# Kernel optimization log

Hardware: AMD Instinct MI355X
Metric: run time of the kernel (lower is better)

## Reference

```python
import jax, jax.numpy as jnp
import numpy as np
import math

STAGE_NUM = 5


def _l2norm(t, axis):
    return t / (1e-6 + jnp.linalg.norm(t, axis=axis, keepdims=True))


def setup_inputs() -> dict:
    key = jax.random.key(0)
    ks = jax.random.split(key, 6)
    b, n, c, h, w, k = 8, 5, 512, 32, 32, 64
    x = jax.random.normal(ks[0], (b, n, c, h, w), dtype=jnp.float32)
    mu = jax.random.normal(ks[1], (1, c, k), dtype=jnp.float32) * math.sqrt(2.0 / k)
    mu = _l2norm(mu, axis=1)
    # 1x1 convs init: normal(0, sqrt(2/(1*1*out_channels)))
    std = math.sqrt(2.0 / c)
    conv1_w = jax.random.normal(ks[2], (c, c), dtype=jnp.float32) * std  # [out,in]
    conv1_b = jnp.zeros((c,), dtype=jnp.float32)
    conv2_w = jax.random.normal(ks[3], (c, c), dtype=jnp.float32) * std
    bn_gamma = jnp.ones((c,), dtype=jnp.float32)
    bn_beta = jnp.zeros((c,), dtype=jnp.float32)
    return {"x": x, "mu": mu, "conv1_w": conv1_w, "conv1_b": conv1_b,
            "conv2_w": conv2_w, "bn_gamma": bn_gamma, "bn_beta": bn_beta}


def reference(x, mu, conv1_w, conv1_b, conv2_w, bn_gamma, bn_beta):
    b, n, c, h, w = x.shape
    xf = x.reshape(b * n, c, h, w)
    idn = xf
    # conv1: 1x1 conv with bias
    y = jnp.einsum('bchw,dc->bdhw', xf, conv1_w) + conv1_b[None, :, None, None]
    # [b, c, N] with N = n*h*w
    y = y.reshape(b, n, c, h, w).transpose(0, 2, 1, 3, 4).reshape(b, c, n * h * w)
    mu_b = jnp.broadcast_to(mu, (b, c, mu.shape[2]))
    z = None
    # EM iterations (no_grad in original; fwd-only so just compute)
    for _ in range(STAGE_NUM):
        z = jax.nn.softmax(jnp.einsum('bcn,bck->bnk', y, mu_b), axis=2)  # [b,N,k]
        z_ = z / (1e-6 + z.sum(axis=1, keepdims=True))
        mu_b = _l2norm(jnp.einsum('bcn,bnk->bck', y, z_), axis=1)
    # reconstruction: mu @ z^T -> [b,c,N]
    rec = jnp.einsum('bck,bnk->bcn', mu_b, z)
    rec = jax.nn.relu(rec.reshape(b, c, n, h, w))
    rec = rec.transpose(0, 2, 1, 3, 4).reshape(b * n, c, h, w)
    # conv2 (no bias) + BatchNorm (training-mode batch stats)
    y2 = jnp.einsum('bchw,dc->bdhw', rec, conv2_w)
    mean = y2.mean(axis=(0, 2, 3), keepdims=True)
    var = y2.var(axis=(0, 2, 3), keepdims=True)
    y2 = (y2 - mean) * jax.lax.rsqrt(var + 1e-5)
    y2 = y2 * bn_gamma[None, :, None, None] + bn_beta[None, :, None, None]
    out = jax.nn.relu(y2 + idn).reshape(b, n, c, h, w)
    return out, mu_b
```

## Files before the change

kernel.cpp:

```cpp
#include <hip/hip_runtime.h>
#include <math.h>

#define CH 512
#define K 64
#define BB 8
#define NIMG 5
#define HW 1024
#define NP 5120
#define BI 40

typedef __attribute__((ext_vector_type(8))) _Float16 f16x8;
typedef __attribute__((ext_vector_type(4))) _Float16 f16x4;
typedef __attribute__((ext_vector_type(4))) float f32x4;
typedef __attribute__((ext_vector_type(8))) short s16x8;

#define AS1 __attribute__((address_space(1)))
#define AS3 __attribute__((address_space(3)))

__device__ inline long mufrag_idx(int b, int c, int k) {
    int cc = c >> 5, l4 = (c >> 3) & 3, e = c & 7;
    int j = k >> 4, l15 = k & 15;
    int lane = l4 * 16 + l15;
    return ((long)b << 15) + (((cc * 4 + j) * 64 + lane) << 3) + e;
}

__global__ __launch_bounds__(256) void wconv(const float* __restrict__ w,
                                             _Float16* __restrict__ o)
{
    int i = blockIdx.x * 256 + threadIdx.x;
    o[i] = (_Float16)w[i];
}

__global__ __launch_bounds__(256) void transpose_f16(
    const float* __restrict__ in, _Float16* __restrict__ out, int P)
{
    __shared__ float tile[64][65];
    int t = threadIdx.x;
    int p0 = blockIdx.x * 64, c0 = blockIdx.y * 64;
    long ibase = (long)blockIdx.z * CH * P;
    long obase = (long)blockIdx.z * P * CH;
    int pl = t & 63, chh = t >> 6;
    #pragma unroll
    for (int i = 0; i < 16; ++i)
        tile[chh + i * 4][pl] = in[ibase + (long)(c0 + chh + i * 4) * P + p0 + pl];
    __syncthreads();
    int cc = t & 31, pr = t >> 5;
    #pragma unroll
    for (int i = 0; i < 8; ++i) {
        int p = pr + i * 8;
        _Float16 lo = (_Float16)tile[cc * 2][p];
        _Float16 hi = (_Float16)tile[cc * 2 + 1][p];
        unsigned lob = (unsigned)*(unsigned short*)&lo;
        unsigned hib = (unsigned)*(unsigned short*)&hi;
        *(unsigned*)&out[obase + (long)(p0 + p) * CH + c0 + cc * 2] = lob | (hib << 16);
    }
}

__global__ __launch_bounds__(256) void bcast_mu2(const float* __restrict__ mu_in,
                                                 float* __restrict__ mu_cur,
                                                 _Float16* __restrict__ muF)
{
    int i = blockIdx.x * 256 + threadIdx.x;
    float v = mu_in[i & 32767];
    mu_cur[i] = v;
    int b = i >> 15, ck = i & 32767, c = ck >> 6, k = ck & 63;
    muF[mufrag_idx(b, c, k)] = (_Float16)v;
}

__global__ __launch_bounds__(256) void conv_tile(
    const _Float16* __restrict__ Wh, const _Float16* __restrict__ inT,
    const float* __restrict__ bias, _Float16* __restrict__ y2h,
    _Float16* __restrict__ y16, _Float16* __restrict__ yT16, int mode)
{
    __shared__ _Float16 Wt[128 * 64];
    __shared__ _Float16 Xt[128 * 64];
    int t = threadIdx.x;
    int lane = t & 63, w = t >> 6;
    int l15 = lane & 15, l4 = lane >> 4;
    int wd = w & 1, wp = w >> 1;
    int sw = (blockIdx.x & 7) * 160 + (blockIdx.x >> 3);
    int px = sw & 7;
    int dy = (sw >> 3) & 3;
    int bi = sw >> 5;
    int d0 = dy * 128;
    int pl0 = px * 128;
    long prow0 = (long)bi * HW + pl0;
    int ci_row = lane >> 3;
    int colb_phys = (lane & 7) * 16;

    f32x4 acc[4][4];
    #pragma unroll
    for (int ai = 0; ai < 4; ++ai)
        #pragma unroll
        for (int bj = 0; bj < 4; ++bj) acc[ai][bj] = (f32x4){0.f, 0.f, 0.f, 0.f};

    for (int c0 = 0; c0 < CH; c0 += 64) {
        __syncthreads();
        #pragma unroll
        for (int i = 0; i < 4; ++i) {
            int row = w * 32 + i * 8 + ci_row;
            int cb = colb_phys ^ ((row & 7) << 4);
            const _Float16* srcW = Wh + (long)(d0 + row) * CH + c0 + (cb >> 1);
            const _Float16* srcX = inT + (prow0 + row) * (long)CH + c0 + (cb >> 1);
            __builtin_amdgcn_global_load_lds((const AS1 void*)srcW,
                (AS3 void*)&Wt[(w * 32 + i * 8) * 64], 16, 0, 0);
            __builtin_amdgcn_global_load_lds((const AS1 void*)srcX,
                (AS3 void*)&Xt[(w * 32 + i * 8) * 64], 16, 0, 0);
        }
        __syncthreads();
        #pragma unroll
        for (int kk = 0; kk < 2; ++kk) {
            f16x8 af[4], bf[4];
            #pragma unroll
            for (int ai = 0; ai < 4; ++ai) {
                int row = wd * 64 + ai * 16 + l15;
                int cb = (kk * 64 + l4 * 16) ^ ((row & 7) << 4);
                af[ai] = *(const f16x8*)((const char*)Wt + row * 128 + cb);
            }
            #pragma unroll
            for (int bj = 0; bj < 4; ++bj) {
                int row = wp * 64 + bj * 16 + l15;
                int cb = (kk * 64 + l4 * 16) ^ ((row & 7) << 4);
                bf[bj] = *(const f16x8*)((const char*)Xt + row * 128 + cb);
            }
            #pragma unroll
            for (int ai = 0; ai < 4; ++ai)
                #pragma unroll
                for (int bj = 0; bj < 4; ++bj)
                    acc[ai][bj] = __builtin_amdgcn_mfma_f32_16x16x32_f16(
                        af[ai], bf[bj], acc[ai][bj], 0, 0, 0);
        }
    }

    int b = bi / NIMG, n = bi % NIMG;
    if (mode == 0) {
        #pragma unroll
        for (int ai = 0; ai < 4; ++ai) {
            int dd = d0 + wd * 64 + ai * 16 + l4 * 4;
            float b0 = bias[dd], b1 = bias[dd + 1], b2 = bias[dd + 2], b3 = bias[dd + 3];
            #pragma unroll
            for (int bj = 0; bj < 4; ++bj) {
                int pb = n * HW + pl0 + wp * 64 + bj * 16 + l15;
                f16x4 pk = { (_Float16)(acc[ai][bj][0] + b0), (_Float16)(acc[ai][bj][1] + b1),
                             (_Float16)(acc[ai][bj][2] + b2), (_Float16)(acc[ai][bj][3] + b3) };
                *(f16x4*)&yT16[((long)b * NP + pb) * CH + dd] = pk;
                long yb = ((long)b * CH + dd) * NP + pb;
                y16[yb] = pk[0];
                y16[yb + NP] = pk[1];
                y16[yb + 2 * NP] = pk[2];
                y16[yb + 3 * NP] = pk[3];
            }
        }
    } else {
        long obase = (long)bi * CH * HW;
        #pragma unroll
        for (int ai = 0; ai < 4; ++ai) {
            int dd = d0 + wd * 64 + ai * 16 + l4 * 4;
            #pragma unroll
            for (int bj = 0; bj < 4; ++bj) {
                int p = pl0 + wp * 64 + bj * 16 + l15;
                long o = obase + (long)dd * HW + p;
                y2h[o] = (_Float16)acc[ai][bj][0];
                y2h[o + HW] = (_Float16)acc[ai][bj][1];
                y2h[o + 2 * HW] = (_Float16)acc[ai][bj][2];
                y2h[o + 3 * HW] = (_Float16)acc[ai][bj][3];
            }
        }
    }
}

__global__ __launch_bounds__(256) void bn_stats2(const _Float16* __restrict__ y2h,
                                                 float* __restrict__ stats,
                                                 float* __restrict__ statsq)
{
    int d = blockIdx.x;
    int t = threadIdx.x;
    float s = 0.f, q = 0.f;
    for (int bi = 0; bi < BI; ++bi) {
        const _Float16* p = y2h + (long)bi * CH * HW + (long)d * HW;
        f16x4 v = *(const f16x4*)&p[t * 4];
        float v0 = (float)v[0], v1 = (float)v[1], v2 = (float)v[2], v3 = (float)v[3];
        s += v0 + v1 + v2 + v3;
        q += v0 * v0 + v1 * v1 + v2 * v2 + v3 * v3;
    }
    #pragma unroll
    for (int off = 1; off < 64; off <<= 1) {
        s += __shfl_xor(s, off, 64);
        q += __shfl_xor(q, off, 64);
    }
    __shared__ float ps[8];
    int wv = t >> 6, ln = t & 63;
    if (ln == 0) { ps[wv] = s; ps[4 + wv] = q; }
    __syncthreads();
    if (t == 0) {
        stats[d]  = ps[0] + ps[1] + ps[2] + ps[3];
        statsq[d] = ps[4] + ps[5] + ps[6] + ps[7];
    }
}

__global__ __launch_bounds__(256) void stage_z_mfma(
    const _Float16* __restrict__ yT, const _Float16* __restrict__ muF,
    _Float16* __restrict__ zT, _Float16* __restrict__ z16,
    float* __restrict__ zsum, int writeZ)
{
    __shared__ float zred[256];
    int t = threadIdx.x;
    int w = t >> 6, lane = t & 63, l15 = lane & 15, l4 = lane >> 4;
    int p0 = blockIdx.x * 64 + w * 16;
    int b = blockIdx.y;
    const _Float16* mf = muF + ((long)b << 15);
    const _Float16* a0p = yT + ((long)b * NP + p0 + l15) * CH + l4 * 8;
    f32x4 acc[4];
    #pragma unroll
    for (int j = 0; j < 4; ++j) acc[j] = (f32x4){0.f, 0.f, 0.f, 0.f};
    #pragma unroll
    for (int cc = 0; cc < 16; ++cc) {
        f16x8 a0 = *(const f16x8*)(a0p + cc * 32);
        #pragma unroll
        for (int j = 0; j < 4; ++j) {
            f16x8 bj = *(const f16x8*)&mf[(((cc * 4 + j) * 64) + lane) * 8];
            acc[j] = __builtin_amdgcn_mfma_f32_16x16x32_f16(a0, bj, acc[j], 0, 0, 0);
        }
    }
    float zv[4][4];
    #pragma unroll
    for (int i = 0; i < 4; ++i) {
        float m = fmaxf(fmaxf(acc[0][i], acc[1][i]), fmaxf(acc[2][i], acc[3][i]));
        #pragma unroll
        for (int off = 1; off < 16; off <<= 1) m = fmaxf(m, __shfl_xor(m, off, 64));
        float e0 = __expf(acc[0][i] - m);
        float e1 = __expf(acc[1][i] - m);
        float e2 = __expf(acc[2][i] - m);
        float e3 = __expf(acc[3][i] - m);
        float s = e0 + e1 + e2 + e3;
        #pragma unroll
        for (int off = 1; off < 16; off <<= 1) s += __shfl_xor(s, off, 64);
        float inv = 1.f / s;
        zv[0][i] = e0 * inv; zv[1][i] = e1 * inv;
        zv[2][i] = e2 * inv; zv[3][i] = e3 * inv;
    }
    int prow = p0 + l4 * 4;
    long ztbase = (long)b * K * NP;
    #pragma unroll
    for (int j = 0; j < 4; ++j) {
        f16x4 pk = { (_Float16)zv[j][0], (_Float16)zv[j][1],
                     (_Float16)zv[j][2], (_Float16)zv[j][3] };
        *(f16x4*)&zT[ztbase + (long)(l15 + 16 * j) * NP + prow] = pk;
    }
    if (writeZ) {
        long zbase = (long)b * NP * K;
        #pragma unroll
        for (int j = 0; j < 4; ++j)
            #pragma unroll
            for (int i = 0; i < 4; ++i)
                z16[zbase + (long)(prow + i) * K + l15 + 16 * j] = (_Float16)zv[j][i];
    }
    float part[4];
    #pragma unroll
    for (int j = 0; j < 4; ++j) {
        part[j] = zv[j][0] + zv[j][1] + zv[j][2] + zv[j][3];
        part[j] += __shfl_xor(part[j], 16, 64);
        part[j] += __shfl_xor(part[j], 32, 64);
    }
    if (l4 == 0) {
        #pragma unroll
        for (int j = 0; j < 4; ++j) zred[w * 64 + l15 + 16 * j] = part[j];
    }
    __syncthreads();
    if (t < 64)
        atomicAdd(&zsum[b * 64 + t], zred[t] + zred[64 + t] + zred[128 + t] + zred[192 + t]);
}

__global__ __launch_bounds__(256) void stage_mu_mfma(
    const _Float16* __restrict__ y16, const _Float16* __restrict__ zT,
    float* __restrict__ macc)
{
    int t = threadIdx.x;
    int w = t >> 6, lane = t & 63, l15 = lane & 15, l4 = lane >> 4;
    int pc = blockIdx.x, ct = blockIdx.y, b = blockIdx.z;
    int c0 = ct * 128 + w * 32;
    int pbase = pc * 320;
    const _Float16* zrow = zT + (long)b * K * NP + (long)l15 * NP + l4 * 8;
    const _Float16* a0p = y16 + ((long)b * CH + c0 + l15) * NP + l4 * 8;
    const _Float16* a1p = y16 + ((long)b * CH + c0 + 16 + l15) * NP + l4 * 8;
    f32x4 acc[2][4];
    #pragma unroll
    for (int ci = 0; ci < 2; ++ci)
        #pragma unroll
        for (int j = 0; j < 4; ++j) acc[ci][j] = (f32x4){0.f, 0.f, 0.f, 0.f};
    for (int p0 = pbase; p0 < pbase + 320; p0 += 32) {
        f16x8 a0 = *(const f16x8*)(a0p + p0);
        f16x8 a1 = *(const f16x8*)(a1p + p0);
        #pragma unroll
        for (int j = 0; j < 4; ++j) {
            f16x8 bj = *(const f16x8*)(zrow + (long)(16 * j) * NP + p0);
            acc[0][j] = __builtin_amdgcn_mfma_f32_16x16x32_f16(a0, bj, acc[0][j], 0, 0, 0);
            acc[1][j] = __builtin_amdgcn_mfma_f32_16x16x32_f16(a1, bj, acc[1][j], 0, 0, 0);
        }
    }
    float* mp = macc + ((long)pc * BB + b) * K * CH;
    #pragma unroll
    for (int ci = 0; ci < 2; ++ci)
        #pragma unroll
        for (int j = 0; j < 4; ++j)
            *(f32x4*)&mp[(long)(l15 + 16 * j) * CH + c0 + ci * 16 + l4 * 4] = acc[ci][j];
}

__global__ __launch_bounds__(256) void mu_norm2(
    const float* __restrict__ macc, const float* __restrict__ zsum,
    float* __restrict__ mu_cur, _Float16* __restrict__ mu16,
    _Float16* __restrict__ muF)
{
    int gw = blockIdx.x * 4 + (threadIdx.x >> 6);
    int lane = threadIdx.x & 63;
    int b = gw >> 6, k = gw & 63;
    float v[8];
    float s = 0.f;
    #pragma unroll
    for (int ci = 0; ci < 8; ++ci) {
        int c = ci * 64 + lane;
        float a = 0.f;
        #pragma unroll
        for (int pcc = 0; pcc < 16; ++pcc)
            a += macc[(((long)pcc * BB + b) * K + k) * CH + c];
        v[ci] = a; s += a * a;
    }
    #pragma unroll
    for (int off = 1; off < 64; off <<= 1) s += __shfl_xor(s, off, 64);
    float d = 1e-6f + zsum[b * 64 + k];
    float scale = 1.f / (1e-6f * d + sqrtf(s));
    long mb = (long)b << 15;
    #pragma unroll
    for (int ci = 0; ci < 8; ++ci) {
        int c = ci * 64 + lane;
        float m = v[ci] * scale;
        mu_cur[mb + (long)c * K + k] = m;
        mu16[mb + (long)c * K + k] = (_Float16)m;
        muF[mufrag_idx(b, c, k)] = (_Float16)m;
    }
}

__global__ __launch_bounds__(256) void rec_mfma(
    const _Float16* __restrict__ z16, const _Float16* __restrict__ mu16,
    _Float16* __restrict__ recT)
{
    __shared__ _Float16 rt[64 * 80];
    int t = threadIdx.x;
    int w = t >> 6, lane = t & 63, l15 = lane & 15, l4 = lane >> 4;
    int p0 = blockIdx.x * 64, ct = blockIdx.y, b = blockIdx.z;
    const _Float16* zb = z16 + (long)b * NP * K;
    const _Float16* mb = mu16 + ((long)b << 15) + (long)(ct * 64 + w * 16 + l15) * K + l4 * 8;
    f32x4 acc[4];
    #pragma unroll
    for (int pj = 0; pj < 4; ++pj) acc[pj] = (f32x4){0.f, 0.f, 0.f, 0.f};
    #pragma unroll
    for (int kc = 0; kc < 64; kc += 32) {
        f16x8 bfr = *(const f16x8*)(mb + kc);
        #pragma unroll
        for (int pj = 0; pj < 4; ++pj) {
            f16x8 a = *(const f16x8*)(zb + (long)(p0 + pj * 16 + l15) * K + kc + l4 * 8);
            acc[pj] = __builtin_amdgcn_mfma_f32_16x16x32_f16(a, bfr, acc[pj], 0, 0, 0);
        }
    }
    #pragma unroll
    for (int pj = 0; pj < 4; ++pj)
        #pragma unroll
        for (int i = 0; i < 4; ++i)
            rt[(pj * 16 + l4 * 4 + i) * 80 + w * 16 + l15] = (_Float16)fmaxf(acc[pj][i], 0.f);
    __syncthreads();
    #pragma unroll
    for (int it = 0; it < 2; ++it) {
        int l = t + it * 256;
        int row = l >> 3, s8 = l & 7;
        *(s16x8*)&recT[((long)b * NP + p0 + row) * CH + ct * 64 + s8 * 8] =
            *(const s16x8*)&rt[row * 80 + s8 * 8];
    }
}

__global__ __launch_bounds__(256) void final_kernel(
    const _Float16* __restrict__ y2h, const float* __restrict__ x,
    const float* __restrict__ stats, const float* __restrict__ statsq,
    const float* __restrict__ gamma, const float* __restrict__ beta,
    const float* __restrict__ mu_cur, float* __restrict__ out)
{
    long i4 = (long)blockIdx.x * 256 + threadIdx.x;
    const long NMAIN4 = (long)BI * CH * HW / 4;
    if (i4 < NMAIN4) {
        long i = i4 * 4;
        int d = (int)((i >> 10) & (CH - 1));
        float s = stats[d], sq = statsq[d];
        const float inv = 1.f / (float)(BI * HW);
        float mean = s * inv;
        float var = sq * inv - mean * mean;
        float rs = rsqrtf(var + 1e-5f);
        float g = rs * gamma[d];
        float bb = beta[d] - mean * g;
        f16x4 yv = *(const f16x4*)&y2h[i];
        float4 xv = *(const float4*)&x[i];
        float4 ov;
        ov.x = fmaxf((float)yv[0] * g + bb + xv.x, 0.f);
        ov.y = fmaxf((float)yv[1] * g + bb + xv.y, 0.f);
        ov.z = fmaxf((float)yv[2] * g + bb + xv.z, 0.f);
        ov.w = fmaxf((float)yv[3] * g + bb + xv.w, 0.f);
        *(float4*)&out[i] = ov;
    } else {
        long j = (i4 - NMAIN4) * 4;
        *(float4*)&out[(long)BI * CH * HW + j] = *(const float4*)&mu_cur[j];
    }
}

extern "C" void kernel_launch(void* const* d_in, const int* in_sizes, int n_in,
                              void* d_out, int out_size, void* d_ws, size_t ws_size,
                              hipStream_t stream) {
    const float* x   = (const float*)d_in[0];
    const float* mu0 = (const float*)d_in[1];
    const float* w1  = (const float*)d_in[2];
    const float* b1  = (const float*)d_in[3];
    const float* w2  = (const float*)d_in[4];
    const float* gm  = (const float*)d_in[5];
    const float* bt  = (const float*)d_in[6];
    float* out = (float*)d_out;

    float* ws = (float*)d_ws;
    _Float16* y16h  = (_Float16*)(ws);
    _Float16* yT16h = (_Float16*)(ws + 10485760);
    _Float16* xTh   = (_Float16*)(ws + 20971520);
    _Float16* zTh   = (_Float16*)(ws + 20971520);
    _Float16* z16h  = (_Float16*)(ws + 22282240);
    _Float16* y2h   = (_Float16*)(ws + 20971520);
    float*    macc  = ws + 27787264 - 4194304;
    float*    mu_cur = ws + 31457280;
    _Float16* Wh1   = (_Float16*)(ws + 31719424);
    _Float16* Wh2   = (_Float16*)(ws + 31850496);
    _Float16* mu16h = (_Float16*)(ws + 31981568);
    _Float16* muFh  = (_Float16*)(ws + 32112640);
    float*    zsum  = ws + 32243712;
    float*    stats = ws + 32246272;
    float*    statsq = ws + 32246784;

    hipMemsetAsync(zsum, 0, 2560 * sizeof(float), stream);

    wconv<<<1024, 256, 0, stream>>>(w1, Wh1);
    wconv<<<1024, 256, 0, stream>>>(w2, Wh2);
    transpose_f16<<<dim3(16, 8, 40), 256, 0, stream>>>(x, xTh, HW);
    conv_tile<<<1280, 256, 0, stream>>>(Wh1, xTh, b1, nullptr, y16h, yT16h, 0);
    bcast_mu2<<<1024, 256, 0, stream>>>(mu0, mu_cur, muFh);

    for (int s = 0; s < 5; ++s) {
        stage_z_mfma<<<dim3(80, 8), 256, 0, stream>>>(yT16h, muFh, zTh, z16h,
                                                      zsum + s * 512, s == 4);
        stage_mu_mfma<<<dim3(16, 4, 8), 256, 0, stream>>>(y16h, zTh, macc);
        mu_norm2<<<128, 256, 0, stream>>>(macc, zsum + s * 512, mu_cur, mu16h, muFh);
    }

    rec_mfma<<<dim3(80, 8, 8), 256, 0, stream>>>(z16h, mu16h, yT16h);
    conv_tile<<<1280, 256, 0, stream>>>(Wh2, yT16h, nullptr, y2h, nullptr, nullptr, 1);
    bn_stats2<<<512, 256, 0, stream>>>(y2h, stats, statsq);
    long total4 = ((long)BI * CH * HW + (long)BB * CH * K) / 4;
    final_kernel<<<(int)((total4 + 255) / 256), 256, 0, stream>>>(
        y2h, x, stats, statsq, gm, bt, mu_cur, out);
}
```

Before: 407.8 us.

## Fuse EM z-softmax and mu accumulation into one kernel per stage

Merges the z-softmax kernel and the mu-accumulation GEMM so each block computes z for 128 pixels, stages it in LDS in MFMA fragment layout, and immediately multiplies it against y to produce partial mu sums. This drops the global zT round trip and one launch per stage. In exchange the grid shrinks to 320 blocks with a large 128-entry accumulator array per thread, which can hurt occupancy. The mu-normalize pass now reduces 40 partials instead of 16, and the z16 buffer moves to a new workspace offset.

```diff
diff --git a/kernel.cpp b/kernel.cpp
--- a/kernel.cpp
+++ b/kernel.cpp
@@ -169,6 +169,192 @@
     }
 }
 
+__global__ __launch_bounds__(256) void zmu_fused(
+    const _Float16* __restrict__ yT, const _Float16* __restrict__ y16,
+    const _Float16* __restrict__ muF, _Float16* __restrict__ z16,
+    float* __restrict__ maccP, float* __restrict__ zsum, int writeZ)
+{
+    __shared__ _Float16 zf[4 * 4 * 64 * 8];
+    __shared__ float zred[256];
+    int t = threadIdx.x;
+    int w = t >> 6, lane = t & 63, l15 = lane & 15, l4 = lane >> 4;
+    int pc = blockIdx.x, b = blockIdx.y;
+    int pblock0 = pc * 128;
+    int p0 = pblock0 + w * 32;
+
+    const _Float16* mf = muF + ((long)b << 15);
+    const _Float16* a0p = yT + ((long)b * NP + p0 + l15) * CH + l4 * 8;
+    const _Float16* a1p = yT + ((long)b * NP + p0 + 16 + l15) * CH + l4 * 8;
+    f32x4 acc[2][4];
+    #pragma unroll
+    for (int pb = 0; pb < 2; ++pb)
+        #pragma unroll
+        for (int j = 0; j < 4; ++j) acc[pb][j] = (f32x4){0.f, 0.f, 0.f, 0.f};
+    #pragma unroll
+    for (int cc = 0; cc < 16; ++cc) {
+        f16x8 a0 = *(const f16x8*)(a0p + cc * 32);
+        f16x8 a1 = *(const f16x8*)(a1p + cc * 32);
+        #pragma unroll
+        for (int j = 0; j < 4; ++j) {
+            f16x8 bj = *(const f16x8*)&mf[(((cc * 4 + j) * 64) + lane) * 8];
+            acc[0][j] = __builtin_amdgcn_mfma_f32_16x16x32_f16(a0, bj, acc[0][j], 0, 0, 0);
+            acc[1][j] = __builtin_amdgcn_mfma_f32_16x16x32_f16(a1, bj, acc[1][j], 0, 0, 0);
+        }
+    }
+    float part[4] = {0.f, 0.f, 0.f, 0.f};
+    long zbase = (long)b * NP * K;
+    #pragma unroll
+    for (int pb = 0; pb < 2; ++pb) {
+        float zv[4][4];
+        #pragma unroll
+        for (int i = 0; i < 4; ++i) {
+            float m = fmaxf(fmaxf(acc[pb][0][i], acc[pb][1][i]),
+                            fmaxf(acc[pb][2][i], acc[pb][3][i]));
+            #pragma unroll
+            for (int off = 1; off < 16; off <<= 1) m = fmaxf(m, __shfl_xor(m, off, 64));
+            float e0 = __expf(acc[pb][0][i] - m);
+            float e1 = __expf(acc[pb][1][i] - m);
+            float e2 = __expf(acc[pb][2][i] - m);
+            float e3 = __expf(acc[pb][3][i] - m);
+            float ss = e0 + e1 + e2 + e3;
+            #pragma unroll
+            for (int off = 1; off < 16; off <<= 1) ss += __shfl_xor(ss, off, 64);
+            float inv = 1.f / ss;
+            zv[0][i] = e0 * inv; zv[1][i] = e1 * inv;
+            zv[2][i] = e2 * inv; zv[3][i] = e3 * inv;
+        }
+        int lanep = (pb * 2 + (l4 >> 1)) * 16 + l15;
+        int e0i = (l4 & 1) * 4;
+        #pragma unroll
+        for (int j = 0; j < 4; ++j) {
+            f16x4 pk = { (_Float16)zv[j][0], (_Float16)zv[j][1],
+                         (_Float16)zv[j][2], (_Float16)zv[j][3] };
+            *(f16x4*)&zf[(((w * 4 + j) * 64 + lanep) << 3) + e0i] = pk;
+        }
+        if (writeZ) {
+            int prow = p0 + pb * 16 + l4 * 4;
+            #pragma unroll
+            for (int j = 0; j < 4; ++j)
+                #pragma unroll
+                for (int i = 0; i < 4; ++i)
+                    z16[zbase + (long)(prow + i) * K + l15 + 16 * j] = (_Float16)zv[j][i];
+        }
+        #pragma unroll
+        for (int j = 0; j < 4; ++j)
+            part[j] += zv[j][0] + zv[j][1] + zv[j][2] + zv[j][3];
+    }
+    #pragma unroll
+    for (int j = 0; j < 4; ++j) {
+        part[j] += __shfl_xor(part[j], 16, 64);
+        part[j] += __shfl_xor(part[j], 32, 64);
+    }
+    if (l4 == 0) {
+        #pragma unroll
+        for (int j = 0; j < 4; ++j) zred[w * 64 + l15 + 16 * j] = part[j];
+    }
+    __syncthreads();
+    if (t < 64)
+        atomicAdd(&zsum[b * 64 + t], zred[t] + zred[64 + t] + zred[128 + t] + zred[192 + t]);
+
+    const _Float16* ybase = y16 + ((long)b * CH + w * 128 + l15) * NP + pblock0 + l4 * 8;
+    f32x4 macc_r[8][4];
+    #pragma unroll
+    for (int r = 0; r < 8; ++r)
+        #pragma unroll
+        for (int j = 0; j < 4; ++j) macc_r[r][j] = (f32x4){0.f, 0.f, 0.f, 0.f};
+    #pragma unroll
+    for (int ps = 0; ps < 4; ++ps) {
+        f16x8 bfr[4];
+        #pragma unroll
+        for (int j = 0; j < 4; ++j)
+            bfr[j] = *(const f16x8*)&zf[((ps * 4 + j) * 64 + lane) << 3];
+        #pragma unroll
+        for (int r = 0; r < 8; ++r) {
+            f16x8 a = *(const f16x8*)(ybase + (long)(r * 16) * NP + ps * 32);
+            #pragma unroll
+            for (int j = 0; j < 4; ++j)
+                macc_r[r][j] = __builtin_amdgcn_mfma_f32_16x16x32_f16(
+                    a, bfr[j], macc_r[r][j], 0, 0, 0);
+        }
+    }
+    float* mp = maccP + ((long)pc * BB + b) * K * CH;
+    #pragma unroll
+    for (int r = 0; r < 8; ++r)
+        #pragma unroll
+        for (int j = 0; j < 4; ++j)
+            *(f32x4*)&mp[(long)(l15 + 16 * j) * CH + w * 128 + r * 16 + l4 * 4] = macc_r[r][j];
+}
+
+__global__ __launch_bounds__(256) void mu_norm3(
+    const float* __restrict__ maccP, const float* __restrict__ zsum,
+    float* __restrict__ mu_cur, _Float16* __restrict__ mu16,
+    _Float16* __restrict__ muF)
+{
+    int gw = blockIdx.x * 4 + (threadIdx.x >> 6);
+    int lane = threadIdx.x & 63;
+    int b = gw >> 6, k = gw & 63;
+    float v[8];
+    float s = 0.f;
+    #pragma unroll
+    for (int ci = 0; ci < 8; ++ci) {
+        int c = ci * 64 + lane;
+        float a = 0.f;
+        for (int pcc = 0; pcc < 40; ++pcc)
+            a += maccP[(((long)pcc * BB + b) * K + k) * CH + c];
+        v[ci] = a; s += a * a;
+    }
+    #pragma unroll
+    for (int off = 1; off < 64; off <<= 1) s += __shfl_xor(s, off, 64);
+    float d = 1e-6f + zsum[b * 64 + k];
+    float scale = 1.f / (1e-6f * d + sqrtf(s));
+    long mb = (long)b << 15;
+    #pragma unroll
+    for (int ci = 0; ci < 8; ++ci) {
+        int c = ci * 64 + lane;
+        float m = v[ci] * scale;
+        mu_cur[mb + (long)c * K + k] = m;
+        mu16[mb + (long)c * K + k] = (_Float16)m;
+        muF[mufrag_idx(b, c, k)] = (_Float16)m;
+    }
+}
+
+__global__ __launch_bounds__(256) void rec_mfma(
+    const _Float16* __restrict__ z16, const _Float16* __restrict__ mu16,
+    _Float16* __restrict__ recT)
+{
+    __shared__ _Float16 rt[64 * 80];
+    int t = threadIdx.x;
+    int w = t >> 6, lane = t & 63, l15 = lane & 15, l4 = lane >> 4;
+    int p0 = blockIdx.x * 64, ct = blockIdx.y, b = blockIdx.z;
+    const _Float16* zb = z16 + (long)b * NP * K;
+    const _Float16* mb = mu16 + ((long)b << 15) + (long)(ct * 64 + w * 16 + l15) * K + l4 * 8;
+    f32x4 acc[4];
+    #pragma unroll
+    for (int pj = 0; pj < 4; ++pj) acc[pj] = (f32x4){0.f, 0.f, 0.f, 0.f};
+    #pragma unroll
+    for (int kc = 0; kc < 64; kc += 32) {
+        f16x8 bfr = *(const f16x8*)(mb + kc);
+        #pragma unroll
+        for (int pj = 0; pj < 4; ++pj) {
+            f16x8 a = *(const f16x8*)(zb + (long)(p0 + pj * 16 + l15) * K + kc + l4 * 8);
+            acc[pj] = __builtin_amdgcn_mfma_f32_16x16x32_f16(a, bfr, acc[pj], 0, 0, 0);
+        }
+    }
+    #pragma unroll
+    for (int pj = 0; pj < 4; ++pj)
+        #pragma unroll
+        for (int i = 0; i < 4; ++i)
+            rt[(pj * 16 + l4 * 4 + i) * 80 + w * 16 + l15] = (_Float16)fmaxf(acc[pj][i], 0.f);
+    __syncthreads();
+    #pragma unroll
+    for (int it = 0; it < 2; ++it) {
+        int l = t + it * 256;
+        int row = l >> 3, s8 = l & 7;
+        *(s16x8*)&recT[((long)b * NP + p0 + row) * CH + ct * 64 + s8 * 8] =
+            *(const s16x8*)&rt[row * 80 + s8 * 8];
+    }
+}
+
 __global__ __launch_bounds__(256) void bn_stats2(const _Float16* __restrict__ y2h,
                                                  float* __restrict__ stats,
                                                  float* __restrict__ statsq)
@@ -195,185 +381,6 @@
     if (t == 0) {
         stats[d]  = ps[0] + ps[1] + ps[2] + ps[3];
         statsq[d] = ps[4] + ps[5] + ps[6] + ps[7];
-    }
-}
-
-__global__ __launch_bounds__(256) void stage_z_mfma(
-    const _Float16* __restrict__ yT, const _Float16* __restrict__ muF,
-    _Float16* __restrict__ zT, _Float16* __restrict__ z16,
-    float* __restrict__ zsum, int writeZ)
-{
-    __shared__ float zred[256];
-    int t = threadIdx.x;
-    int w = t >> 6, lane = t & 63, l15 = lane & 15, l4 = lane >> 4;
-    int p0 = blockIdx.x * 64 + w * 16;
-    int b = blockIdx.y;
-    const _Float16* mf = muF + ((long)b << 15);
-    const _Float16* a0p = yT + ((long)b * NP + p0 + l15) * CH + l4 * 8;
-    f32x4 acc[4];
-    #pragma unroll
-    for (int j = 0; j < 4; ++j) acc[j] = (f32x4){0.f, 0.f, 0.f, 0.f};
-    #pragma unroll
-    for (int cc = 0; cc < 16; ++cc) {
-        f16x8 a0 = *(const f16x8*)(a0p + cc * 32);
-        #pragma unroll
-        for (int j = 0; j < 4; ++j) {
-            f16x8 bj = *(const f16x8*)&mf[(((cc * 4 + j) * 64) + lane) * 8];
-            acc[j] = __builtin_amdgcn_mfma_f32_16x16x32_f16(a0, bj, acc[j], 0, 0, 0);
-        }
-    }
-    float zv[4][4];
-    #pragma unroll
-    for (int i = 0; i < 4; ++i) {
-        float m = fmaxf(fmaxf(acc[0][i], acc[1][i]), fmaxf(acc[2][i], acc[3][i]));
-        #pragma unroll
-        for (int off = 1; off < 16; off <<= 1) m = fmaxf(m, __shfl_xor(m, off, 64));
-        float e0 = __expf(acc[0][i] - m);
-        float e1 = __expf(acc[1][i] - m);
-        float e2 = __expf(acc[2][i] - m);
-        float e3 = __expf(acc[3][i] - m);
-        float s = e0 + e1 + e2 + e3;
-        #pragma unroll
-        for (int off = 1; off < 16; off <<= 1) s += __shfl_xor(s, off, 64);
-        float inv = 1.f / s;
-        zv[0][i] = e0 * inv; zv[1][i] = e1 * inv;
-        zv[2][i] = e2 * inv; zv[3][i] = e3 * inv;
-    }
-    int prow = p0 + l4 * 4;
-    long ztbase = (long)b * K * NP;
-    #pragma unroll
-    for (int j = 0; j < 4; ++j) {
-        f16x4 pk = { (_Float16)zv[j][0], (_Float16)zv[j][1],
-                     (_Float16)zv[j][2], (_Float16)zv[j][3] };
-        *(f16x4*)&zT[ztbase + (long)(l15 + 16 * j) * NP + prow] = pk;
-    }
-    if (writeZ) {
-        long zbase = (long)b * NP * K;
-        #pragma unroll
-        for (int j = 0; j < 4; ++j)
-            #pragma unroll
-            for (int i = 0; i < 4; ++i)
-                z16[zbase + (long)(prow + i) * K + l15 + 16 * j] = (_Float16)zv[j][i];
-    }
-    float part[4];
-    #pragma unroll
-    for (int j = 0; j < 4; ++j) {
-        part[j] = zv[j][0] + zv[j][1] + zv[j][2] + zv[j][3];
-        part[j] += __shfl_xor(part[j], 16, 64);
-        part[j] += __shfl_xor(part[j], 32, 64);
-    }
-    if (l4 == 0) {
-        #pragma unroll
-        for (int j = 0; j < 4; ++j) zred[w * 64 + l15 + 16 * j] = part[j];
-    }
-    __syncthreads();
-    if (t < 64)
-        atomicAdd(&zsum[b * 64 + t], zred[t] + zred[64 + t] + zred[128 + t] + zred[192 + t]);
-}
-
-__global__ __launch_bounds__(256) void stage_mu_mfma(
-    const _Float16* __restrict__ y16, const _Float16* __restrict__ zT,
-    float* __restrict__ macc)
-{
-    int t = threadIdx.x;
-    int w = t >> 6, lane = t & 63, l15 = lane & 15, l4 = lane >> 4;
-    int pc = blockIdx.x, ct = blockIdx.y, b = blockIdx.z;
-    int c0 = ct * 128 + w * 32;
-    int pbase = pc * 320;
-    const _Float16* zrow = zT + (long)b * K * NP + (long)l15 * NP + l4 * 8;
-    const _Float16* a0p = y16 + ((long)b * CH + c0 + l15) * NP + l4 * 8;
-    const _Float16* a1p = y16 + ((long)b * CH + c0 + 16 + l15) * NP + l4 * 8;
-    f32x4 acc[2][4];
-    #pragma unroll
-    for (int ci = 0; ci < 2; ++ci)
-        #pragma unroll
-        for (int j = 0; j < 4; ++j) acc[ci][j] = (f32x4){0.f, 0.f, 0.f, 0.f};
-    for (int p0 = pbase; p0 < pbase + 320; p0 += 32) {
-        f16x8 a0 = *(const f16x8*)(a0p + p0);
-        f16x8 a1 = *(const f16x8*)(a1p + p0);
-        #pragma unroll
-        for (int j = 0; j < 4; ++j) {
-            f16x8 bj = *(const f16x8*)(zrow + (long)(16 * j) * NP + p0);
-            acc[0][j] = __builtin_amdgcn_mfma_f32_16x16x32_f16(a0, bj, acc[0][j], 0, 0, 0);
-            acc[1][j] = __builtin_amdgcn_mfma_f32_16x16x32_f16(a1, bj, acc[1][j], 0, 0, 0);
-        }
-    }
-    float* mp = macc + ((long)pc * BB + b) * K * CH;
-    #pragma unroll
-    for (int ci = 0; ci < 2; ++ci)
-        #pragma unroll
-        for (int j = 0; j < 4; ++j)
-            *(f32x4*)&mp[(long)(l15 + 16 * j) * CH + c0 + ci * 16 + l4 * 4] = acc[ci][j];
-}
-
-__global__ __launch_bounds__(256) void mu_norm2(
-    const float* __restrict__ macc, const float* __restrict__ zsum,
-    float* __restrict__ mu_cur, _Float16* __restrict__ mu16,
-    _Float16* __restrict__ muF)
-{
-    int gw = blockIdx.x * 4 + (threadIdx.x >> 6);
-    int lane = threadIdx.x & 63;
-    int b = gw >> 6, k = gw & 63;
-    float v[8];
-    float s = 0.f;
-    #pragma unroll
-    for (int ci = 0; ci < 8; ++ci) {
-        int c = ci * 64 + lane;
-        float a = 0.f;
-        #pragma unroll
-        for (int pcc = 0; pcc < 16; ++pcc)
-            a += macc[(((long)pcc * BB + b) * K + k) * CH + c];
-        v[ci] = a; s += a * a;
-    }
-    #pragma unroll
-    for (int off = 1; off < 64; off <<= 1) s += __shfl_xor(s, off, 64);
-    float d = 1e-6f + zsum[b * 64 + k];
-    float scale = 1.f / (1e-6f * d + sqrtf(s));
-    long mb = (long)b << 15;
-    #pragma unroll
-    for (int ci = 0; ci < 8; ++ci) {
-        int c = ci * 64 + lane;
-        float m = v[ci] * scale;
-        mu_cur[mb + (long)c * K + k] = m;
-        mu16[mb + (long)c * K + k] = (_Float16)m;
-        muF[mufrag_idx(b, c, k)] = (_Float16)m;
-    }
-}
-
-__global__ __launch_bounds__(256) void rec_mfma(
-    const _Float16* __restrict__ z16, const _Float16* __restrict__ mu16,
-    _Float16* __restrict__ recT)
-{
-    __shared__ _Float16 rt[64 * 80];
-    int t = threadIdx.x;
-    int w = t >> 6, lane = t & 63, l15 = lane & 15, l4 = lane >> 4;
-    int p0 = blockIdx.x * 64, ct = blockIdx.y, b = blockIdx.z;
-    const _Float16* zb = z16 + (long)b * NP * K;
-    const _Float16* mb = mu16 + ((long)b << 15) + (long)(ct * 64 + w * 16 + l15) * K + l4 * 8;
-    f32x4 acc[4];
-    #pragma unroll
-    for (int pj = 0; pj < 4; ++pj) acc[pj] = (f32x4){0.f, 0.f, 0.f, 0.f};
-    #pragma unroll
-    for (int kc = 0; kc < 64; kc += 32) {
-        f16x8 bfr = *(const f16x8*)(mb + kc);
-        #pragma unroll
-        for (int pj = 0; pj < 4; ++pj) {
-            f16x8 a = *(const f16x8*)(zb + (long)(p0 + pj * 16 + l15) * K + kc + l4 * 8);
-            acc[pj] = __builtin_amdgcn_mfma_f32_16x16x32_f16(a, bfr, acc[pj], 0, 0, 0);
-        }
-    }
-    #pragma unroll
-    for (int pj = 0; pj < 4; ++pj)
-        #pragma unroll
-        for (int i = 0; i < 4; ++i)
-            rt[(pj * 16 + l4 * 4 + i) * 80 + w * 16 + l15] = (_Float16)fmaxf(acc[pj][i], 0.f);
-    __syncthreads();
-    #pragma unroll
-    for (int it = 0; it < 2; ++it) {
-        int l = t + it * 256;
-        int row = l >> 3, s8 = l & 7;
-        *(s16x8*)&recT[((long)b * NP + p0 + row) * CH + ct * 64 + s8 * 8] =
-            *(const s16x8*)&rt[row * 80 + s8 * 8];
     }
 }
 
@@ -425,10 +432,8 @@
     _Float16* y16h  = (_Float16*)(ws);
     _Float16* yT16h = (_Float16*)(ws + 10485760);
     _Float16* xTh   = (_Float16*)(ws + 20971520);
-    _Float16* zTh   = (_Float16*)(ws + 20971520);
-    _Float16* z16h  = (_Float16*)(ws + 22282240);
+    float*    maccP = ws + 20971520;
     _Float16* y2h   = (_Float16*)(ws + 20971520);
-    float*    macc  = ws + 27787264 - 4194304;
     float*    mu_cur = ws + 31457280;
     _Float16* Wh1   = (_Float16*)(ws + 31719424);
     _Float16* Wh2   = (_Float16*)(ws + 31850496);
@@ -437,6 +442,7 @@
     float*    zsum  = ws + 32243712;
     float*    stats = ws + 32246272;
     float*    statsq = ws + 32246784;
+    _Float16* z16h  = (_Float16*)(ws + 32247296);
 
     hipMemsetAsync(zsum, 0, 2560 * sizeof(float), stream);
 
@@ -447,10 +453,9 @@
     bcast_mu2<<<1024, 256, 0, stream>>>(mu0, mu_cur, muFh);
 
     for (int s = 0; s < 5; ++s) {
-        stage_z_mfma<<<dim3(80, 8), 256, 0, stream>>>(yT16h, muFh, zTh, z16h,
-                                                      zsum + s * 512, s == 4);
-        stage_mu_mfma<<<dim3(16, 4, 8), 256, 0, stream>>>(y16h, zTh, macc);
-        mu_norm2<<<128, 256, 0, stream>>>(macc, zsum + s * 512, mu_cur, mu16h, muFh);
+        zmu_fused<<<dim3(40, 8), 256, 0, stream>>>(yT16h, y16h, muFh, z16h,
+                                                   maccP, zsum + s * 512, s == 4);
+        mu_norm3<<<128, 256, 0, stream>>>(maccP, zsum + s * 512, mu_cur, mu16h, muFh);
     }
 
     rec_mfma<<<dim3(80, 8, 8), 256, 0, stream>>>(z16h, mu16h, yT16h);
```

Result: slower. 474.1 us (+16.3%).
